# Optimization experiments

Measured on AMD Instinct MI355X. Metric: run time of the kernel, lower is better.

Reference implementation:

```python
import jax, jax.numpy as jnp
import numpy as np
import math

NH = 4  # num_heads


def _mab(Q, K, wq, bq, wk, bk, wv, bv, wo, bo):
    """MAB from the original code, RE='None', ln=False, numlayers=1.
    NOTE: softmax scale is sqrt(dim_V) (full model dim), as in the source."""
    D = wq.shape[1]
    dh = D // NH
    Qp = Q @ wq + bq                      # [B,Sq,D]
    Kp = K @ wk + bk                      # [B,Sk,D]
    Vp = K @ wv + bv                      # [B,Sk,D]
    B, Sq, _ = Qp.shape
    Sk = Kp.shape[1]
    Qh = Qp.reshape(B, Sq, NH, dh)
    Kh = Kp.reshape(B, Sk, NH, dh)
    Vh = Vp.reshape(B, Sk, NH, dh)
    A = jax.nn.softmax(jnp.einsum('bqhd,bkhd->bhqk', Qh, Kh) / math.sqrt(D), axis=-1)
    O = (Qh + jnp.einsum('bhqk,bkhd->bqhd', A, Vh)).reshape(B, Sq, D)
    return O + jax.nn.relu(O @ wo + bo)   # resO + relu(fc_o(O))


def _isab(X, I, m0, m1):
    B = X.shape[0]
    H = _mab(jnp.broadcast_to(I, (B,) + I.shape[1:]), X, *m0)
    return _mab(X, H, *m1)


def setup_inputs() -> dict:
    key = jax.random.key(0)
    ks = iter(jax.random.split(key, 64))

    def p(*shape):
        return jax.random.normal(next(ks), shape, jnp.float32) * 0.05

    B, S = 4096, 64
    Dv, De, Dw, Dh, M = 256, 256, 64, 128, 4
    return dict(
        v=jax.random.normal(next(ks), (B, S, Dv), jnp.float32),
        W=jax.random.normal(next(ks), (B, S, Dw), jnp.float32),
        Q=jax.random.normal(next(ks), (B, 1, De), jnp.float32),
        pe_w=p(Dw, Dv), pe_b=p(Dv),
        i1_I=p(1, M, Dh),
        i1_m0_wq=p(Dh, Dh), i1_m0_bq=p(Dh), i1_m0_wk=p(Dv, Dh), i1_m0_bk=p(Dh),
        i1_m0_wv=p(Dv, Dh), i1_m0_bv=p(Dh), i1_m0_wo=p(Dh, Dh), i1_m0_bo=p(Dh),
        i1_m1_wq=p(Dv, Dh), i1_m1_bq=p(Dh), i1_m1_wk=p(Dh, Dh), i1_m1_bk=p(Dh),
        i1_m1_wv=p(Dh, Dh), i1_m1_bv=p(Dh), i1_m1_wo=p(Dh, Dh), i1_m1_bo=p(Dh),
        i2_I=p(1, M, Dh),
        i2_m0_wq=p(Dh, Dh), i2_m0_bq=p(Dh), i2_m0_wk=p(Dh, Dh), i2_m0_bk=p(Dh),
        i2_m0_wv=p(Dh, Dh), i2_m0_bv=p(Dh), i2_m0_wo=p(Dh, Dh), i2_m0_bo=p(Dh),
        i2_m1_wq=p(Dh, Dh), i2_m1_bq=p(Dh), i2_m1_wk=p(Dh, Dh), i2_m1_bk=p(Dh),
        i2_m1_wv=p(Dh, Dh), i2_m1_bv=p(Dh), i2_m1_wo=p(Dh, Dh), i2_m1_bo=p(Dh),
        dec_wq=p(De, Dh), dec_bq=p(Dh), dec_wk=p(Dh, Dh), dec_bk=p(Dh),
        dec_wv=p(Dh, Dh), dec_bv=p(Dh), dec_wo=p(Dh, Dh), dec_bo=p(Dh),
        out_w=p(Dh, De), out_b=p(De),
    )


def reference(v, W, Q, pe_w, pe_b,
              i1_I, i1_m0_wq, i1_m0_bq, i1_m0_wk, i1_m0_bk, i1_m0_wv, i1_m0_bv, i1_m0_wo, i1_m0_bo,
              i1_m1_wq, i1_m1_bq, i1_m1_wk, i1_m1_bk, i1_m1_wv, i1_m1_bv, i1_m1_wo, i1_m1_bo,
              i2_I, i2_m0_wq, i2_m0_bq, i2_m0_wk, i2_m0_bk, i2_m0_wv, i2_m0_bv, i2_m0_wo, i2_m0_bo,
              i2_m1_wq, i2_m1_bq, i2_m1_wk, i2_m1_bk, i2_m1_wv, i2_m1_bv, i2_m1_wo, i2_m1_bo,
              dec_wq, dec_bq, dec_wk, dec_bk, dec_wv, dec_bv, dec_wo, dec_bo,
              out_w, out_b):
    # RankAdd: v = v + pe_v(W)
    v = v + W @ pe_w + pe_b
    # enc_v: two ISAB blocks (dropout p=0.0)
    v = _isab(v, i1_I,
              (i1_m0_wq, i1_m0_bq, i1_m0_wk, i1_m0_bk, i1_m0_wv, i1_m0_bv, i1_m0_wo, i1_m0_bo),
              (i1_m1_wq, i1_m1_bq, i1_m1_wk, i1_m1_bk, i1_m1_wv, i1_m1_bv, i1_m1_wo, i1_m1_bo))
    v = _isab(v, i2_I,
              (i2_m0_wq, i2_m0_bq, i2_m0_wk, i2_m0_bk, i2_m0_wv, i2_m0_bv, i2_m0_wo, i2_m0_bo),
              (i2_m1_wq, i2_m1_bq, i2_m1_wk, i2_m1_bk, i2_m1_wv, i2_m1_bv, i2_m1_wo, i2_m1_bo))
    # dec_v: PrevQ MAB(Q, v) then Linear(dim_hidden -> output_edim)
    o = _mab(Q, v, dec_wq, dec_bq, dec_wk, dec_bk, dec_wv, dec_bv, dec_wo, dec_bo)
    return o @ out_w + out_b  # [B, 1, output_edim]
```

## Files before the change

kernel.cpp:

```cpp
#include <hip/hip_runtime.h>
#include <hip/hip_bf16.h>

typedef unsigned short u16;
typedef unsigned int u32;
typedef __attribute__((ext_vector_type(8))) short short8;
typedef __attribute__((ext_vector_type(4))) float f32x4;

#define DEVI static __device__ __forceinline__

DEVI u16 f2b(float f) {
    union { float f; unsigned v; } x; x.f = f;
    unsigned r = x.v + 0x7fffu + ((x.v >> 16) & 1u);
    return (u16)(r >> 16);
}
DEVI float b2f(u16 u) { union { unsigned v; float f; } x; x.v = ((unsigned)u) << 16; return x.f; }

#define MFMA(a, b, c) __builtin_amdgcn_mfma_f32_16x16x32_bf16((a), (b), (c), 0, 0, 0)

#define RW_PEW     0
#define RW_I1M0_WK 16384
#define RW_I1M0_WV 49152
#define RW_I1M1_WQ 81920
#define RW_I1M1_WO 114688
#define RW_I2M0_WK 131072
#define RW_I2M0_WV 147456
#define RW_I2M1_WQ 163840
#define RW_I2M1_WO 180224
#define RW_DEC_WK  196608
#define RW_DEC_WV  212992
#define RW_END     229376

#define FT_I1M0_WO 0
#define FT_I2M0_WO 16384
#define FT_I1M1_WK 32768
#define FT_I1M1_WV 49152
#define FT_I2M1_WK 65536
#define FT_I2M1_WV 81920
#define FT_DEC_WO  98304
#define FT_DEC_WQ  114688
#define FT_OUT_W   147456
#define FT_END     180224

#define PA 136
#define PT 68
#define SCALE 0.08838834764831845f

struct Params {
    const float* in[49];
    const u16* wrep;
    const float* ft;
    const float* qpre;
    float* out;
};

struct RepArgs {
    const float* src[11];
    const float* tsrc[9];
    u16* dst;
    float* fdst;
    float* qpre;
    const float* I1; const float* wq1; const float* bq1;
    const float* I2; const float* wq2; const float* bq2;
};

__global__ void repack_kernel(RepArgs a) {
    const int offs[11] = {RW_PEW, RW_I1M0_WK, RW_I1M0_WV, RW_I1M1_WQ, RW_I1M1_WO,
                          RW_I2M0_WK, RW_I2M0_WV, RW_I2M1_WQ, RW_I2M1_WO, RW_DEC_WK, RW_DEC_WV};
    const int Ks[11] = {64, 256, 256, 256, 128, 128, 128, 128, 128, 128, 128};
    const int Ns[11] = {256, 128, 128, 128, 128, 128, 128, 128, 128, 128, 128};
    int t = blockIdx.x * 256 + threadIdx.x;
    if (t < 28672) {
        int m = 0, u = t;
        for (m = 0; m < 11; ++m) {
            int un = (Ks[m] * Ns[m]) >> 3;
            if (u < un) break;
            u -= un;
        }
        int l = u & 63, f = u >> 6;
        int ksteps = Ks[m] >> 5;
        int nt = f / ksteps, ks = f - nt * ksteps;
        int N = Ns[m];
        const float* s = a.src[m] + (ks * 32 + (l >> 4) * 8) * N + nt * 16 + (l & 15);
        u16* d = a.dst + offs[m] + ((f * 64 + l) << 3);
        short8 v;
        #pragma unroll
        for (int j = 0; j < 8; ++j) v[j] = (short)f2b(s[j * N]);
        *(short8*)d = v;
    } else if (t < 51200) {
        const int TK[9] = {128, 128, 128, 128, 128, 128, 128, 256, 128};
        const int TN[9] = {128, 128, 128, 128, 128, 128, 128, 128, 256};
        const int TOFF[9] = {FT_I1M0_WO, FT_I2M0_WO, FT_I1M1_WK, FT_I1M1_WV,
                             FT_I2M1_WK, FT_I2M1_WV, FT_DEC_WO, FT_DEC_WQ, FT_OUT_W};
        int u = t - 28672;
        int m = 0;
        for (m = 0; m < 9; ++m) {
            int un = (TK[m] * TN[m]) >> 3;
            if (u < un) break;
            u -= un;
        }
        int K = TK[m], N = TN[m];
        int kc = K >> 3;
        int n = u / kc, k0 = (u - n * kc) << 3;
        const float* s = a.tsrc[m] + k0 * N + n;
        float* d = a.fdst + TOFF[m] + n * K + k0;
        f32x4 v0, v1;
        #pragma unroll
        for (int j = 0; j < 4; ++j) v0[j] = s[j * N];
        #pragma unroll
        for (int j = 0; j < 4; ++j) v1[j] = s[(4 + j) * N];
        *(f32x4*)d = v0;
        *(f32x4*)(d + 4) = v1;
    } else {
        int q_t = t - 51200;
        int which = q_t >> 9, q = (q_t >> 7) & 3, n = q_t & 127;
        const float* I  = which ? a.I2  : a.I1;
        const float* wq = which ? a.wq2 : a.wq1;
        const float* bq = which ? a.bq2 : a.bq1;
        float acc = bq[n];
        for (int k = 0; k < 128; ++k) acc += I[q * 128 + k] * wq[k * 128 + n];
        a.qpre[q_t] = acc;
    }
}

template <int MODE>
DEVI void gemm128(const u16* A, const u16* __restrict__ Brep,
                  const float* __restrict__ bias, u16* out, int tid) {
    int l = tid & 63, w = tid >> 6;
    int lr = l & 15, lq = l >> 4;
    int Mt = w & 3, Ntb = (w >> 2) * 4;
    f32x4 z = {0.f, 0.f, 0.f, 0.f};
    f32x4 acc[4];
    #pragma unroll
    for (int i = 0; i < 4; ++i) acc[i] = z;
    const u16* arow = A + (Mt * 16 + lr) * PA + lq * 8;
    #pragma unroll
    for (int ks = 0; ks < 4; ++ks) {
        short8 af = *(const short8*)(arow + ks * 32);
        #pragma unroll
        for (int i = 0; i < 4; ++i) {
            int nt = Ntb + i;
            short8 bfr = *(const short8*)(Brep + (((nt << 2) + ks) * 64 + l) * 8);
            acc[i] = MFMA(af, bfr, acc[i]);
        }
    }
    #pragma unroll
    for (int i = 0; i < 4; ++i) {
        int col = (Ntb + i) * 16 + lr;
        float bv = bias[col];
        #pragma unroll
        for (int r = 0; r < 4; ++r) {
            int row = Mt * 16 + lq * 4 + r;
            float v = acc[i][r] + bv;
            if (MODE == 2) v = b2f(A[row * PA + col]) + fmaxf(v, 0.f);
            if (MODE == 1) out[col * PT + row] = f2b(v);
            else           out[row * PA + col] = f2b(v);
        }
    }
}

DEVI void att_m0(const float* __restrict__ qpre, const float* __restrict__ woT,
                 const float* __restrict__ bo, const u16* KT, const u16* V,
                 float* sS, float* SCR, int tid) {
    #pragma unroll
    for (int ii = 0; ii < 2; ++ii) {
        int idx = tid + ii * 512;
        int h = idx >> 8, q = (idx >> 6) & 3, k = idx & 63;
        const float* qp = qpre + q * 128 + h * 32;
        const u16* kp = KT + (h * 32) * PT + k;
        float s = 0.f;
        #pragma unroll
        for (int d8 = 0; d8 < 8; ++d8) {
            f32x4 q4 = *(const f32x4*)(qp + d8 * 4);
            #pragma unroll
            for (int j = 0; j < 4; ++j) s += q4[j] * b2f(kp[(d8 * 4 + j) * PT]);
        }
        sS[(h * 4 + q) * 64 + k] = s * SCALE;
    }
    __syncthreads();
    {
        int w = tid >> 6, l = tid & 63;
        int row = w * 2 + (l >> 5);
        int j = (l & 31) * 2;
        float e0 = sS[row * 64 + j], e1 = sS[row * 64 + j + 1];
        float m = fmaxf(e0, e1);
        #pragma unroll
        for (int off = 1; off < 32; off <<= 1) m = fmaxf(m, __shfl_xor(m, off));
        e0 = __expf(e0 - m); e1 = __expf(e1 - m);
        float su = e0 + e1;
        #pragma unroll
        for (int off = 1; off < 32; off <<= 1) su += __shfl_xor(su, off);
        float inv = 1.f / su;
        sS[row * 64 + j] = e0 * inv;
        sS[row * 64 + j + 1] = e1 * inv;
    }
    __syncthreads();
    {
        int q = tid & 3, n = tid >> 2, h = n >> 5;
        float o = qpre[q * 128 + n];
        const float* ar = sS + (h * 4 + q) * 64;
        #pragma unroll 8
        for (int k8 = 0; k8 < 16; ++k8) {
            f32x4 a4 = *(const f32x4*)(ar + k8 * 4);
            #pragma unroll
            for (int j = 0; j < 4; ++j) o += a4[j] * b2f(V[(k8 * 4 + j) * PA + n]);
        }
        SCR[n * 4 + q] = o;
    }
    __syncthreads();
    if (tid < 256) {
        int n = tid & 127, c = tid >> 7;
        const float* wp = woT + n * 128 + c * 64;
        f32x4 acc = {0.f, 0.f, 0.f, 0.f};
        #pragma unroll 4
        for (int k4 = 0; k4 < 16; ++k4) {
            f32x4 w4 = *(const f32x4*)(wp + k4 * 4);
            #pragma unroll
            for (int j = 0; j < 4; ++j) {
                f32x4 o4 = *(const f32x4*)(SCR + (c * 64 + k4 * 4 + j) * 4);
                acc[0] += o4[0] * w4[j]; acc[1] += o4[1] * w4[j];
                acc[2] += o4[2] * w4[j]; acc[3] += o4[3] * w4[j];
            }
        }
        *(f32x4*)(sS + c * 512 + n * 4) = acc;
    }
    __syncthreads();
    {
        int q = tid & 3, n = tid >> 2;
        float val = sS[n * 4 + q] + sS[512 + n * 4 + q] + bo[n];
        SCR[512 + n * 4 + q] = SCR[n * 4 + q] + fmaxf(val, 0.f);
    }
    __syncthreads();
}

DEVI void att_m1(const u16* Qp, const float* __restrict__ wkT, const float* __restrict__ bk,
                 const float* __restrict__ wvT, const float* __restrict__ bv,
                 u16* Oout, float* sS, float* SCR, int tid) {
    const float* HT = SCR + 512;
    float* K2 = SCR + 1024;
    float* V2 = SCR + 1536;
    if (tid < 256) {
        int n = tid & 127, half = tid >> 7;
        const float* wp = (half ? wvT : wkT) + n * 128;
        const float* bsel = half ? bv : bk;
        f32x4 acc = {0.f, 0.f, 0.f, 0.f};
        #pragma unroll 4
        for (int j4 = 0; j4 < 32; ++j4) {
            f32x4 w4 = *(const f32x4*)(wp + j4 * 4);
            #pragma unroll
            for (int j = 0; j < 4; ++j) {
                f32x4 h4 = *(const f32x4*)(HT + (j4 * 4 + j) * 4);
                acc[0] += h4[0] * w4[j]; acc[1] += h4[1] * w4[j];
                acc[2] += h4[2] * w4[j]; acc[3] += h4[3] * w4[j];
            }
        }
        float bb = bsel[n];
        float* dst = half ? V2 : K2;
        dst[0 * 128 + n] = acc[0] + bb; dst[1 * 128 + n] = acc[1] + bb;
        dst[2 * 128 + n] = acc[2] + bb; dst[3 * 128 + n] = acc[3] + bb;
    }
    __syncthreads();
    if (tid < 256) {
        int h = tid >> 6, q = tid & 63;
        const u16* qrow = Qp + q * PA + h * 32;
        const float* kb = K2 + h * 32;
        f32x4 s = {0.f, 0.f, 0.f, 0.f};
        #pragma unroll
        for (int d8 = 0; d8 < 4; ++d8) {
            short8 q8 = *(const short8*)(qrow + d8 * 8);
            f32x4 kra[4], krb[4];
            #pragma unroll
            for (int c = 0; c < 4; ++c) {
                kra[c] = *(const f32x4*)(kb + c * 128 + d8 * 8);
                krb[c] = *(const f32x4*)(kb + c * 128 + d8 * 8 + 4);
            }
            #pragma unroll
            for (int j = 0; j < 4; ++j) {
                float qv = b2f((u16)q8[j]);
                s[0] += qv * kra[0][j]; s[1] += qv * kra[1][j];
                s[2] += qv * kra[2][j]; s[3] += qv * kra[3][j];
            }
            #pragma unroll
            for (int j = 0; j < 4; ++j) {
                float qv = b2f((u16)q8[4 + j]);
                s[0] += qv * krb[0][j]; s[1] += qv * krb[1][j];
                s[2] += qv * krb[2][j]; s[3] += qv * krb[3][j];
            }
        }
        float s0 = s[0] * SCALE, s1 = s[1] * SCALE, s2 = s[2] * SCALE, s3 = s[3] * SCALE;
        float m = fmaxf(fmaxf(s0, s1), fmaxf(s2, s3));
        s0 = __expf(s0 - m); s1 = __expf(s1 - m); s2 = __expf(s2 - m); s3 = __expf(s3 - m);
        float inv = 1.f / (s0 + s1 + s2 + s3);
        f32x4 a; a[0] = s0 * inv; a[1] = s1 * inv; a[2] = s2 * inv; a[3] = s3 * inv;
        *(f32x4*)(sS + (h * 64 + q) * 4) = a;
    }
    __syncthreads();
    #pragma unroll
    for (int ii = 0; ii < 16; ++ii) {
        int idx = tid + ii * 512;
        int q = idx >> 7, n = idx & 127, h = n >> 5;
        f32x4 a4 = *(const f32x4*)(sS + (h * 64 + q) * 4);
        float o = b2f(Qp[q * PA + n]);
        o += a4[0] * V2[0 * 128 + n] + a4[1] * V2[1 * 128 + n]
           + a4[2] * V2[2 * 128 + n] + a4[3] * V2[3 * 128 + n];
        Oout[q * PA + n] = f2b(o);
    }
    __syncthreads();
}

__global__ __launch_bounds__(512, 4) void fused_kernel(Params P) {
    __shared__ __align__(16) u16 R0[128 * PT];
    __shared__ __align__(16) u16 R1[64 * PA];
    __shared__ __align__(16) u16 R2[64 * PA];
    __shared__ __align__(16) float sS[1024];
    __shared__ __align__(16) float SCR[2048];

    const int b = blockIdx.x;
    const int tid = threadIdx.x;
    const int l = tid & 63, w = tid >> 6;
    const int lr = l & 15, lq = l >> 4;
    const int Mt = w & 3, Ntb = (w >> 2) * 4;

    {
        u32* z0 = (u32*)R0;
        for (int i = tid; i < 4352; i += 512) z0[i] = 0;
        u32* z1 = (u32*)R1;
        for (int i = tid; i < 4352; i += 512) z1[i] = 0;
        u32* z2 = (u32*)R2;
        for (int i = tid; i < 4352; i += 512) z2[i] = 0;
        for (int i = tid; i < 1024; i += 512) sS[i] = 0.f;
        for (int i = tid; i < 2048; i += 512) SCR[i] = 0.f;
    }
    __syncthreads();

    const float* v_in = P.in[0] + b * (64 * 256);
    const float* W_in = P.in[1] + b * (64 * 64);
    const float* Q_in = P.in[2] + b * 256;
    const float* ft = P.ft;

    f32x4 z = {0.f, 0.f, 0.f, 0.f};
    f32x4 aK[4], aV[4], aQ[4];
    #pragma unroll
    for (int i = 0; i < 4; ++i) { aK[i] = z; aV[i] = z; aQ[i] = z; }

    u16* sVh = R0;
    const float* wrow = W_in + (Mt * 16 + lr) * 64 + lq * 8;
    #pragma unroll 1
    for (int p = 0; p < 2; ++p) {
        f32x4 ar[4];
        #pragma unroll
        for (int i = 0; i < 4; ++i) ar[i] = z;
        #pragma unroll
        for (int ks = 0; ks < 2; ++ks) {
            f32x4 w0 = *(const f32x4*)(wrow + ks * 32);
            f32x4 w1 = *(const f32x4*)(wrow + ks * 32 + 4);
            short8 af;
            #pragma unroll
            for (int j = 0; j < 4; ++j) { af[j] = (short)f2b(w0[j]); af[4 + j] = (short)f2b(w1[j]); }
            #pragma unroll
            for (int i = 0; i < 4; ++i) {
                int ntg = p * 8 + Ntb + i;
                short8 bfr = *(const short8*)(P.wrep + RW_PEW + ((ntg * 2 + ks) * 64 + l) * 8);
                ar[i] = MFMA(af, bfr, ar[i]);
            }
        }
        __syncthreads();
        #pragma unroll
        for (int i = 0; i < 4; ++i) {
            int ntl = Ntb + i;
            int coll = ntl * 16 + lr;
            int colg = p * 128 + coll;
            float pb = P.in[4][colg];
            #pragma unroll
            for (int r = 0; r < 4; ++r) {
                int row = Mt * 16 + lq * 4 + r;
                sVh[row * PA + coll] = f2b(ar[i][r] + pb + v_in[row * 256 + colg]);
            }
        }
        __syncthreads();
        #pragma unroll
        for (int ks = 0; ks < 4; ++ks) {
            short8 af = *(const short8*)(sVh + (Mt * 16 + lr) * PA + ks * 32 + lq * 8);
            int kk = p * 4 + ks;
            #pragma unroll
            for (int i = 0; i < 4; ++i) {
                int nt = Ntb + i;
                short8 b0 = *(const short8*)(P.wrep + RW_I1M0_WK + ((nt * 8 + kk) * 64 + l) * 8);
                aK[i] = MFMA(af, b0, aK[i]);
                short8 b1 = *(const short8*)(P.wrep + RW_I1M0_WV + ((nt * 8 + kk) * 64 + l) * 8);
                aV[i] = MFMA(af, b1, aV[i]);
                short8 b2v = *(const short8*)(P.wrep + RW_I1M1_WQ + ((nt * 8 + kk) * 64 + l) * 8);
                aQ[i] = MFMA(af, b2v, aQ[i]);
            }
        }
        __syncthreads();
    }
    #pragma unroll
    for (int i = 0; i < 4; ++i) {
        int col = (Ntb + i) * 16 + lr;
        float bkv = P.in[9][col];
        float bvv = P.in[11][col];
        float bqv = P.in[15][col];
        #pragma unroll
        for (int r = 0; r < 4; ++r) {
            int row = Mt * 16 + lq * 4 + r;
            R0[col * PT + row] = f2b(aK[i][r] + bkv);
            R1[row * PA + col] = f2b(aV[i][r] + bvv);
            R2[row * PA + col] = f2b(aQ[i][r] + bqv);
        }
    }
    __syncthreads();

    att_m0(P.qpre, ft + FT_I1M0_WO, P.in[13], R0, R1, sS, SCR, tid);
    att_m1(R2, ft + FT_I1M1_WK, P.in[17], ft + FT_I1M1_WV, P.in[19],
           R0, sS, SCR, tid);
    gemm128<2>(R0, P.wrep + RW_I1M1_WO, P.in[21], R1, tid);
    __syncthreads();
    gemm128<1>(R1, P.wrep + RW_I2M0_WK, P.in[26], R0, tid);
    gemm128<0>(R1, P.wrep + RW_I2M0_WV, P.in[28], R2, tid);
    __syncthreads();
    att_m0(P.qpre + 512, ft + FT_I2M0_WO, P.in[30], R0, R2, sS, SCR, tid);
    gemm128<0>(R1, P.wrep + RW_I2M1_WQ, P.in[32], R2, tid);
    __syncthreads();
    att_m1(R2, ft + FT_I2M1_WK, P.in[34], ft + FT_I2M1_WV, P.in[36],
           R0, sS, SCR, tid);
    gemm128<2>(R0, P.wrep + RW_I2M1_WO, P.in[38], R1, tid);
    __syncthreads();
    gemm128<1>(R1, P.wrep + RW_DEC_WK, P.in[42], R0, tid);
    gemm128<0>(R1, P.wrep + RW_DEC_WV, P.in[44], R2, tid);
    __syncthreads();

    {
        int n = tid & 127, c = tid >> 7;
        const float* wp = ft + FT_DEC_WQ + n * 256 + c * 64;
        const float* qq = Q_in + c * 64;
        float acc = 0.f;
        #pragma unroll 8
        for (int k4 = 0; k4 < 16; ++k4) {
            f32x4 w4 = *(const f32x4*)(wp + k4 * 4);
            f32x4 q4 = *(const f32x4*)(qq + k4 * 4);
            acc += q4[0] * w4[0] + q4[1] * w4[1] + q4[2] * w4[2] + q4[3] * w4[3];
        }
        sS[c * 128 + n] = acc;
    }
    __syncthreads();
    if (tid < 128) {
        SCR[tid] = sS[tid] + sS[128 + tid] + sS[256 + tid] + sS[384 + tid] + P.in[40][tid];
    }
    __syncthreads();
    if (tid < 256) {
        int h = tid >> 6, k = tid & 63;
        const float* qd = SCR + h * 32;
        const u16* kp = R0 + (h * 32) * PT + k;
        float s = 0.f;
        #pragma unroll
        for (int d8 = 0; d8 < 8; ++d8) {
            f32x4 q4 = *(const f32x4*)(qd + d8 * 4);
            #pragma unroll
            for (int j = 0; j < 4; ++j) s += q4[j] * b2f(kp[(d8 * 4 + j) * PT]);
        }
        sS[h * 64 + k] = s * SCALE;
    }
    __syncthreads();
    if (w < 4) {
        float v = sS[w * 64 + l];
        float m = v;
        #pragma unroll
        for (int off = 1; off < 64; off <<= 1) m = fmaxf(m, __shfl_xor(m, off));
        v = __expf(v - m);
        float su = v;
        #pragma unroll
        for (int off = 1; off < 64; off <<= 1) su += __shfl_xor(su, off);
        sS[w * 64 + l] = v / su;
    }
    __syncthreads();
    if (tid < 128) {
        int n = tid, h = n >> 5;
        float o = SCR[n];
        const float* arr = sS + h * 64;
        #pragma unroll 8
        for (int k8 = 0; k8 < 16; ++k8) {
            f32x4 a4 = *(const f32x4*)(arr + k8 * 4);
            #pragma unroll
            for (int j = 0; j < 4; ++j) o += a4[j] * b2f(R2[(k8 * 4 + j) * PA + n]);
        }
        SCR[128 + n] = o;
    }
    __syncthreads();
    if (tid < 256) {
        int n = tid & 127, c = tid >> 7;
        const float* wp = ft + FT_DEC_WO + n * 128 + c * 64;
        const float* ov = SCR + 128 + c * 64;
        float acc = 0.f;
        #pragma unroll 8
        for (int k4 = 0; k4 < 16; ++k4) {
            f32x4 w4 = *(const f32x4*)(wp + k4 * 4);
            f32x4 o4 = *(const f32x4*)(ov + k4 * 4);
            acc += o4[0] * w4[0] + o4[1] * w4[1] + o4[2] * w4[2] + o4[3] * w4[3];
        }
        sS[256 + c * 128 + n] = acc;
    }
    __syncthreads();
    if (tid < 128) {
        float val = sS[256 + tid] + sS[384 + tid] + P.in[46][tid];
        SCR[256 + tid] = SCR[128 + tid] + fmaxf(val, 0.f);
    }
    __syncthreads();
    {
        int j = tid & 255, c = tid >> 8;
        const float* wp = ft + FT_OUT_W + j * 128 + c * 64;
        const float* ov = SCR + 256 + c * 64;
        float acc = 0.f;
        #pragma unroll 8
        for (int k4 = 0; k4 < 16; ++k4) {
            f32x4 w4 = *(const f32x4*)(wp + k4 * 4);
            f32x4 o4 = *(const f32x4*)(ov + k4 * 4);
            acc += o4[0] * w4[0] + o4[1] * w4[1] + o4[2] * w4[2] + o4[3] * w4[3];
        }
        sS[c * 256 + j] = acc;
    }
    __syncthreads();
    if (tid < 256) {
        P.out[b * 256 + tid] = sS[tid] + sS[256 + tid] + P.in[48][tid];
    }
}

extern "C" void kernel_launch(void* const* d_in, const int* in_sizes, int n_in,
                              void* d_out, int out_size, void* d_ws, size_t ws_size,
                              hipStream_t stream) {
    RepArgs ra;
    const int srcidx[11] = {3, 8, 10, 14, 20, 25, 27, 31, 37, 41, 43};
    for (int i = 0; i < 11; ++i) ra.src[i] = (const float*)d_in[srcidx[i]];
    const int tidx[9] = {12, 29, 16, 18, 33, 35, 45, 39, 47};
    for (int i = 0; i < 9; ++i) ra.tsrc[i] = (const float*)d_in[tidx[i]];
    ra.dst = (u16*)d_ws;
    ra.fdst = (float*)((char*)d_ws + RW_END * 2);
    ra.qpre = ra.fdst + FT_END;
    ra.I1 = (const float*)d_in[5];  ra.wq1 = (const float*)d_in[6];  ra.bq1 = (const float*)d_in[7];
    ra.I2 = (const float*)d_in[22]; ra.wq2 = (const float*)d_in[23]; ra.bq2 = (const float*)d_in[24];
    repack_kernel<<<204, 256, 0, stream>>>(ra);

    Params P;
    for (int i = 0; i < 49; ++i) P.in[i] = (const float*)d_in[i];
    P.wrep = (const u16*)d_ws;
    P.ft = (const float*)((char*)d_ws + RW_END * 2);
    P.qpre = P.ft + FT_END;
    P.out = (float*)d_out;
    fused_kernel<<<4096, 512, 0, stream>>>(P);
}
```

Measured before the change: 1.401 ms.

## Drop LDS padding and scratch buffer by aliasing into dead tiles, remove zero-init

Removes the padding on the LDS tile strides (PA 136→128, PT 68→64) and the separate 8 KB SCR scratch array. Scratch data now lives in the dead regions of R0 and R1, and the upfront zeroing of all shared buffers is dropped. The aim is a smaller LDS footprint and less setup work, which could allow more resident blocks, though launch_bounds min-blocks drops from 4 to 3. Without padding, the strided column accesses through PT and PA are likely to hit LDS bank conflicts, and the aliasing relies on those tiles being dead at each point of reuse.

```diff
diff --git a/kernel.cpp b/kernel.cpp
--- a/kernel.cpp
+++ b/kernel.cpp
@@ -41,8 +41,8 @@
 #define FT_OUT_W   147456
 #define FT_END     180224
 
-#define PA 136
-#define PT 68
+#define PA 128
+#define PT 64
 #define SCALE 0.08838834764831845f
 
 struct Params {
@@ -160,7 +160,7 @@
 
 DEVI void att_m0(const float* __restrict__ qpre, const float* __restrict__ woT,
                  const float* __restrict__ bo, const u16* KT, const u16* V,
-                 float* sS, float* SCR, int tid) {
+                 float* scr, float* sS, int tid) {
     #pragma unroll
     for (int ii = 0; ii < 2; ++ii) {
         int idx = tid + ii * 512;
@@ -204,7 +204,7 @@
             #pragma unroll
             for (int j = 0; j < 4; ++j) o += a4[j] * b2f(V[(k8 * 4 + j) * PA + n]);
         }
-        SCR[n * 4 + q] = o;
+        scr[n * 4 + q] = o;
     }
     __syncthreads();
     if (tid < 256) {
@@ -216,7 +216,7 @@
             f32x4 w4 = *(const f32x4*)(wp + k4 * 4);
             #pragma unroll
             for (int j = 0; j < 4; ++j) {
-                f32x4 o4 = *(const f32x4*)(SCR + (c * 64 + k4 * 4 + j) * 4);
+                f32x4 o4 = *(const f32x4*)(scr + (c * 64 + k4 * 4 + j) * 4);
                 acc[0] += o4[0] * w4[j]; acc[1] += o4[1] * w4[j];
                 acc[2] += o4[2] * w4[j]; acc[3] += o4[3] * w4[j];
             }
@@ -227,17 +227,14 @@
     {
         int q = tid & 3, n = tid >> 2;
         float val = sS[n * 4 + q] + sS[512 + n * 4 + q] + bo[n];
-        SCR[512 + n * 4 + q] = SCR[n * 4 + q] + fmaxf(val, 0.f);
+        scr[512 + n * 4 + q] = scr[n * 4 + q] + fmaxf(val, 0.f);
     }
     __syncthreads();
 }
 
 DEVI void att_m1(const u16* Qp, const float* __restrict__ wkT, const float* __restrict__ bk,
                  const float* __restrict__ wvT, const float* __restrict__ bv,
-                 u16* Oout, float* sS, float* SCR, int tid) {
-    const float* HT = SCR + 512;
-    float* K2 = SCR + 1024;
-    float* V2 = SCR + 1536;
+                 u16* Oout, float* kv, const float* HT, float* sS, int tid) {
     if (tid < 256) {
         int n = tid & 127, half = tid >> 7;
         const float* wp = (half ? wvT : wkT) + n * 128;
@@ -254,7 +251,7 @@
             }
         }
         float bb = bsel[n];
-        float* dst = half ? V2 : K2;
+        float* dst = kv + half * 512;
         dst[0 * 128 + n] = acc[0] + bb; dst[1 * 128 + n] = acc[1] + bb;
         dst[2 * 128 + n] = acc[2] + bb; dst[3 * 128 + n] = acc[3] + bb;
     }
@@ -262,7 +259,7 @@
     if (tid < 256) {
         int h = tid >> 6, q = tid & 63;
         const u16* qrow = Qp + q * PA + h * 32;
-        const float* kb = K2 + h * 32;
+        const float* kb = kv + h * 32;
         f32x4 s = {0.f, 0.f, 0.f, 0.f};
         #pragma unroll
         for (int d8 = 0; d8 < 4; ++d8) {
@@ -300,37 +297,26 @@
         int q = idx >> 7, n = idx & 127, h = n >> 5;
         f32x4 a4 = *(const f32x4*)(sS + (h * 64 + q) * 4);
         float o = b2f(Qp[q * PA + n]);
-        o += a4[0] * V2[0 * 128 + n] + a4[1] * V2[1 * 128 + n]
-           + a4[2] * V2[2 * 128 + n] + a4[3] * V2[3 * 128 + n];
+        o += a4[0] * kv[512 + 0 * 128 + n] + a4[1] * kv[512 + 1 * 128 + n]
+           + a4[2] * kv[512 + 2 * 128 + n] + a4[3] * kv[512 + 3 * 128 + n];
         Oout[q * PA + n] = f2b(o);
     }
     __syncthreads();
 }
 
-__global__ __launch_bounds__(512, 4) void fused_kernel(Params P) {
+__global__ __launch_bounds__(512, 3) void fused_kernel(Params P) {
     __shared__ __align__(16) u16 R0[128 * PT];
     __shared__ __align__(16) u16 R1[64 * PA];
     __shared__ __align__(16) u16 R2[64 * PA];
     __shared__ __align__(16) float sS[1024];
-    __shared__ __align__(16) float SCR[2048];
+    float* R0f = (float*)R0;
+    float* R1f = (float*)R1;
 
     const int b = blockIdx.x;
     const int tid = threadIdx.x;
     const int l = tid & 63, w = tid >> 6;
     const int lr = l & 15, lq = l >> 4;
     const int Mt = w & 3, Ntb = (w >> 2) * 4;
-
-    {
-        u32* z0 = (u32*)R0;
-        for (int i = tid; i < 4352; i += 512) z0[i] = 0;
-        u32* z1 = (u32*)R1;
-        for (int i = tid; i < 4352; i += 512) z1[i] = 0;
-        u32* z2 = (u32*)R2;
-        for (int i = tid; i < 4352; i += 512) z2[i] = 0;
-        for (int i = tid; i < 1024; i += 512) sS[i] = 0.f;
-        for (int i = tid; i < 2048; i += 512) SCR[i] = 0.f;
-    }
-    __syncthreads();
 
     const float* v_in = P.in[0] + b * (64 * 256);
     const float* W_in = P.in[1] + b * (64 * 64);
@@ -410,19 +396,19 @@
     }
     __syncthreads();
 
-    att_m0(P.qpre, ft + FT_I1M0_WO, P.in[13], R0, R1, sS, SCR, tid);
+    att_m0(P.qpre, ft + FT_I1M0_WO, P.in[13], R0, R1, R0f, sS, tid);
     att_m1(R2, ft + FT_I1M1_WK, P.in[17], ft + FT_I1M1_WV, P.in[19],
-           R0, sS, SCR, tid);
+           R0, R1f, R0f + 512, sS, tid);
     gemm128<2>(R0, P.wrep + RW_I1M1_WO, P.in[21], R1, tid);
     __syncthreads();
     gemm128<1>(R1, P.wrep + RW_I2M0_WK, P.in[26], R0, tid);
     gemm128<0>(R1, P.wrep + RW_I2M0_WV, P.in[28], R2, tid);
     __syncthreads();
-    att_m0(P.qpre + 512, ft + FT_I2M0_WO, P.in[30], R0, R2, sS, SCR, tid);
+    att_m0(P.qpre + 512, ft + FT_I2M0_WO, P.in[30], R0, R2, R0f, sS, tid);
     gemm128<0>(R1, P.wrep + RW_I2M1_WQ, P.in[32], R2, tid);
     __syncthreads();
     att_m1(R2, ft + FT_I2M1_WK, P.in[34], ft + FT_I2M1_WV, P.in[36],
-           R0, sS, SCR, tid);
+           R0, R1f, R0f + 512, sS, tid);
     gemm128<2>(R0, P.wrep + RW_I2M1_WO, P.in[38], R1, tid);
     __syncthreads();
     gemm128<1>(R1, P.wrep + RW_DEC_WK, P.in[42], R0, tid);
@@ -444,12 +430,12 @@
     }
     __syncthreads();
     if (tid < 128) {
-        SCR[tid] = sS[tid] + sS[128 + tid] + sS[256 + tid] + sS[384 + tid] + P.in[40][tid];
+        R1f[tid] = sS[tid] + sS[128 + tid] + sS[256 + tid] + sS[384 + tid] + P.in[40][tid];
     }
     __syncthreads();
     if (tid < 256) {
         int h = tid >> 6, k = tid & 63;
-        const float* qd = SCR + h * 32;
+        const float* qd = R1f + h * 32;
         const u16* kp = R0 + (h * 32) * PT + k;
         float s = 0.f;
         #pragma unroll
@@ -475,7 +461,7 @@
     __syncthreads();
     if (tid < 128) {
         int n = tid, h = n >> 5;
-        float o = SCR[n];
+        float o = R1f[n];
         const float* arr = sS + h * 64;
         #pragma unroll 8
         for (int k8 = 0; k8 < 16; ++k8) {
@@ -483,13 +469,13 @@
             #pragma unroll
             for (int j = 0; j < 4; ++j) o += a4[j] * b2f(R2[(k8 * 4 + j) * PA + n]);
         }
-        SCR[128 + n] = o;
+        R1f[128 + n] = o;
     }
     __syncthreads();
     if (tid < 256) {
         int n = tid & 127, c = tid >> 7;
         const float* wp = ft + FT_DEC_WO + n * 128 + c * 64;
-        const float* ov = SCR + 128 + c * 64;
+        const float* ov = R1f + 128 + c * 64;
         float acc = 0.f;
         #pragma unroll 8
         for (int k4 = 0; k4 < 16; ++k4) {
@@ -502,13 +488,13 @@
     __syncthreads();
     if (tid < 128) {
         float val = sS[256 + tid] + sS[384 + tid] + P.in[46][tid];
-        SCR[256 + tid] = SCR[128 + tid] + fmaxf(val, 0.f);
+        R1f[256 + tid] = R1f[128 + tid] + fmaxf(val, 0.f);
     }
     __syncthreads();
     {
         int j = tid & 255, c = tid >> 8;
         const float* wp = ft + FT_OUT_W + j * 128 + c * 64;
-        const float* ov = SCR + 256 + c * 64;
+        const float* ov = R1f + 256 + c * 64;
         float acc = 0.f;
         #pragma unroll 8
         for (int k4 = 0; k4 < 16; ++k4) {
```

New measurement: 1.514 ms. +8.1%, slower.
